# Optimization experiments

Measured on AMD Instinct MI355X. Metric: run time of the kernel, lower is better.

The kernel has to match this reference:

```python
import jax, jax.numpy as jnp
import numpy as np

N = 20000      # points
K = 16         # neighbor pairs per query per branch
M = N * K      # total pairs
C = 384        # embed_dim
H = 6          # num_heads
HD = C // H    # head_dim = 64
H1 = H // 2    # cartesian-branch heads
L = 24         # quant_grid_length (window 6.0 / quant 0.25)
Q = 0.25       # quant_size
LS = 24        # quant_grid_length_sphere (120 / 5)
QS = 5.0       # quant_size_sphere
A = 0.05 * 0.25  # exponential_split 'a'
SCALE = HD ** -0.5


def setup_inputs() -> dict:
    key = jax.random.key(0)
    ks = jax.random.split(key, 12)
    s = 0.02
    inp = {}
    inp["query_feats"] = jax.random.normal(ks[0], (N, C), jnp.float32)
    inp["xyz"] = jax.random.uniform(ks[1], (N, 3), jnp.float32, -3.0, 3.0)
    inp["index_0"] = jnp.repeat(jnp.arange(N, dtype=jnp.int32), K)
    inp["index_1"] = jax.random.randint(ks[2], (M,), 0, N, dtype=jnp.int32)
    inp["index_0_sphere"] = jnp.repeat(jnp.arange(N, dtype=jnp.int32), K)
    inp["index_1_sphere"] = jax.random.randint(ks[3], (M,), 0, N, dtype=jnp.int32)
    inp["W_qkv"] = jax.random.normal(ks[4], (C, 3 * C), jnp.float32) * s
    inp["b_qkv"] = jnp.zeros((3 * C,), jnp.float32)
    inp["W_proj"] = jax.random.normal(ks[5], (C, C), jnp.float32) * s
    inp["b_proj"] = jnp.zeros((C,), jnp.float32)
    inp["tq"] = jax.random.normal(ks[6], (2 * L - 1, 3, H1, HD), jnp.float32) * s
    inp["tk"] = jax.random.normal(ks[7], (2 * L - 1, 3, H1, HD), jnp.float32) * s
    inp["tv"] = jax.random.normal(ks[8], (2 * L - 1, 3, H1, HD), jnp.float32) * s
    inp["tq_s"] = jax.random.normal(ks[9], (2 * LS, 3, H - H1, HD), jnp.float32) * s
    inp["tk_s"] = jax.random.normal(ks[10], (2 * LS, 3, H - H1, HD), jnp.float32) * s
    inp["tv_s"] = jax.random.normal(ks[11], (2 * LS, 3, H - H1, HD), jnp.float32) * s
    return inp


def _cart2sphere(xyz):
    x, y, z = xyz[:, 0], xyz[:, 1], xyz[:, 2]
    theta = (jnp.arctan2(y, x) + np.pi) * (180.0 / np.pi)
    beta = jnp.arctan2(jnp.sqrt(x * x + y * y), z) * (180.0 / np.pi)
    r = jnp.sqrt(x * x + y * y + z * z)
    return jnp.stack([theta, beta, r], -1)


def _rel_idx_cart(xyz, i0, i1):
    rel = xyz[i0] - xyz[i1]  # [M,3]
    idx = jnp.floor(rel / Q).astype(jnp.int32) + (L - 1)
    return jnp.clip(idx, 0, 2 * L - 2)


def _rel_idx_sphere(sph, i0, i1):
    rel = sph[i0] - sph[i1]  # [M,3] (theta, beta, r)
    idx01 = jnp.clip(jnp.floor(rel[:, :2] / QS).astype(jnp.int32) + LS, 0, 2 * LS - 1)
    # exponential_split on radial dim
    r = rel[:, 2]
    ra = jnp.abs(r)
    flag = (r >= 0).astype(jnp.float32)
    idx = 2.0 * jnp.floor(jnp.log((ra + 2.0 * A) / A) / np.log(2.0)) - 2.0
    idx = idx + ((3.0 * jnp.exp2(jnp.floor(idx / 2.0)) - 2.0) * A <= ra).astype(jnp.float32)
    idx = idx * (2.0 * flag - 1.0) + (flag - 1.0)
    idx2 = jnp.clip(idx.astype(jnp.int32) + 24, 0, 2 * LS - 1)
    return jnp.concatenate([idx01, idx2[:, None]], 1)


def _branch(q, k, v, i0, i1, rel_idx, Tq, Tk, Tv):
    # q,k,v: [N,h,d]; i0/i1: [M]; rel_idx: [M,3]; tables: [R,3,h,d]
    qg = q[i0]  # [M,h,d]
    kg = k[i1]
    attn = jnp.einsum('mhd,mhd->mh', qg, kg)
    for dim in range(3):
        attn = attn + jnp.einsum('mhd,mhd->mh', qg, Tq[rel_idx[:, dim], dim])
        attn = attn + jnp.einsum('mhd,mhd->mh', kg, Tk[rel_idx[:, dim], dim])
    # segment softmax over queries (i0)
    seg_max = jax.ops.segment_max(attn, i0, num_segments=N)
    ex = jnp.exp(attn - seg_max[i0])
    p = ex / jax.ops.segment_sum(ex, i0, num_segments=N)[i0]  # [M,h]
    vg = v[i1] + Tv[rel_idx[:, 0], 0] + Tv[rel_idx[:, 1], 1] + Tv[rel_idx[:, 2], 2]
    return jax.ops.segment_sum(p[:, :, None] * vg, i0, num_segments=N)  # [N,h,d]


def reference(query_feats, xyz, index_0, index_1, index_0_sphere, index_1_sphere,
              W_qkv, b_qkv, W_proj, b_proj, tq, tk, tv, tq_s, tk_s, tv_s):
    i0 = index_0.astype(jnp.int32)
    i1 = index_1.astype(jnp.int32)
    i0s = index_0_sphere.astype(jnp.int32)
    i1s = index_1_sphere.astype(jnp.int32)
    qkv = (query_feats @ W_qkv + b_qkv).reshape(N, 3, H, HD)
    q = qkv[:, 0] * SCALE
    k = qkv[:, 1]
    v = qkv[:, 2]
    sph = _cart2sphere(xyz)
    ri = _rel_idx_cart(xyz, i0, i1)
    out1 = _branch(q[:, :H1], k[:, :H1], v[:, :H1], i0, i1, ri, tq, tk, tv)
    ri_s = _rel_idx_sphere(sph, i0s, i1s)
    out2 = _branch(q[:, H1:], k[:, H1:], v[:, H1:], i0s, i1s, ri_s, tq_s, tk_s, tv_s)
    x = jnp.concatenate([out1, out2], 1).reshape(N, C)
    return x @ W_proj + b_proj
```

## Files before the change

kernel.cpp:

```cpp
#include <hip/hip_runtime.h>
#include <hip/hip_bf16.h>

namespace {

constexpr int NP   = 20000;
constexpr int CD   = 384;
constexpr int QKVD = 1152;
constexpr int TC   = 47 * 3 * 3 * 64;
constexpr int TS   = 48 * 3 * 3 * 64;

constexpr int PB0 = NP * CD / 4 / 256;
constexpr int PB1 = PB0 + (QKVD / 32) * (CD / 32);
constexpr int PB2 = PB1 + (CD / 32) * (CD / 32);
constexpr int PB3 = PB2 + 27 * 7;

typedef __attribute__((ext_vector_type(8))) short short8;
typedef __attribute__((ext_vector_type(4))) float f32x4;
typedef __attribute__((ext_vector_type(2))) float f32x2;

__device__ inline float f32_atan2(float y, float x) {
  return (float)atan2((double)y, (double)x);
}
__device__ inline float f32_log(float x) {
  return (float)log((double)x);
}

__device__ inline float bfl(unsigned u) {
  union { unsigned u; float f; } c; c.u = u << 16; return c.f;
}
__device__ inline float bfh(unsigned u) {
  union { unsigned u; float f; } c; c.u = u & 0xffff0000u; return c.f;
}
__device__ inline f32x2 up2(unsigned u) {
  f32x2 r;
  r.x = bfl(u);
  r.y = bfh(u);
  return r;
}
__device__ inline unsigned short f2bf(float x) {
  __hip_bfloat16 hb = __float2bfloat16(x);
  unsigned short u; __builtin_memcpy(&u, &hb, 2);
  return u;
}

#if __has_builtin(__builtin_amdgcn_fdot2_f32_bf16)
#define HAVE_BF16_DOT 1
typedef __attribute__((ext_vector_type(2))) __bf16 bf16x2_t;
__device__ inline float dot2bf(unsigned a, unsigned b, float c) {
  bf16x2_t av, bv;
  __builtin_memcpy(&av, &a, 4);
  __builtin_memcpy(&bv, &b, 4);
  return __builtin_amdgcn_fdot2_f32_bf16(av, bv, c, false);
}
#endif

__device__ inline void async16(const void* g, void* l) {
  __builtin_amdgcn_global_load_lds(
      (const __attribute__((address_space(1))) unsigned int*)g,
      (__attribute__((address_space(3))) unsigned int*)l,
      16, 0, 0);
}

__global__ __launch_bounds__(256) void prep_all_k(const float* __restrict__ qf,
                                                  unsigned short* __restrict__ qf_b,
                                                  const float* __restrict__ Wqkv,
                                                  unsigned short* __restrict__ wqkvT,
                                                  const float* __restrict__ Wproj,
                                                  unsigned short* __restrict__ wprojT,
                                                  const float* __restrict__ tq,
                                                  const float* __restrict__ tk,
                                                  const float* __restrict__ tv,
                                                  const float* __restrict__ tqs,
                                                  const float* __restrict__ tks,
                                                  const float* __restrict__ tvs,
                                                  unsigned short* __restrict__ tq_b,
                                                  unsigned short* __restrict__ tk_b,
                                                  unsigned short* __restrict__ tv_b,
                                                  unsigned short* __restrict__ tqs_b,
                                                  unsigned short* __restrict__ tks_b,
                                                  unsigned short* __restrict__ tvs_b,
                                                  const float* __restrict__ xyz,
                                                  float* __restrict__ sph) {
  const int bid = blockIdx.x;
  const int tid = threadIdx.x;
  __shared__ float t[32][33];

  if (bid < PB0) {
    int i = (bid * 256 + tid) * 4;
    float4 v = *(const float4*)(qf + i);
    ushort4 o;
    o.x = f2bf(v.x); o.y = f2bf(v.y); o.z = f2bf(v.z); o.w = f2bf(v.w);
    *(ushort4*)(qf_b + i) = o;
  } else if (bid < PB2) {
    const float* in;
    unsigned short* out;
    int R, Cc, bx, by;
    if (bid < PB1) {
      in = Wqkv; out = wqkvT; R = CD; Cc = QKVD;
      int tt = bid - PB0; bx = tt % (QKVD / 32); by = tt / (QKVD / 32);
    } else {
      in = Wproj; out = wprojT; R = CD; Cc = CD;
      int tt = bid - PB1; bx = tt % (CD / 32); by = tt / (CD / 32);
    }
    const int c0 = bx * 32, r0 = by * 32;
    const int tx = tid & 31, ty = tid >> 5;
    #pragma unroll
    for (int i = 0; i < 32; i += 8)
      t[ty + i][tx] = in[(size_t)(r0 + ty + i) * Cc + (c0 + tx)];
    __syncthreads();
    #pragma unroll
    for (int i = 0; i < 32; i += 8)
      out[(size_t)(c0 + ty + i) * R + (r0 + tx)] = f2bf(t[tx][ty + i]);
  } else {
    const int tt = bid - PB2;
    const int bx = tt % 27, y = tt / 27;
    const int th = bx * 256 + tid;
    if (y < 6) {
      const float* in = (y == 0) ? tq : (y == 1) ? tk : (y == 2) ? tv
                      : (y == 3) ? tqs : (y == 4) ? tks : tvs;
      unsigned short* out = (y == 0) ? tq_b : (y == 1) ? tk_b : (y == 2) ? tv_b
                          : (y == 3) ? tqs_b : (y == 4) ? tks_b : tvs_b;
      const int n = (y < 3) ? TC : TS;
      int i = th * 4;
      if (i < n) {
        float4 v = *(const float4*)(in + i);
        ushort4 o;
        o.x = f2bf(v.x); o.y = f2bf(v.y); o.z = f2bf(v.z); o.w = f2bf(v.w);
        *(ushort4*)(out + i) = o;
      }
    } else {
#pragma clang fp contract(off)
      #pragma unroll
      for (int r = 0; r < 4; ++r) {
        int i = th * 4 + r;
        if (i < NP) {
          const float PIF = 3.14159265358979323846f;
          const float R2D = 57.29577951308232f;
          float x = xyz[i * 3 + 0], yy = xyz[i * 3 + 1], z = xyz[i * 3 + 2];
          float sxy = x * x + yy * yy;
          sph[i * 3 + 0] = (f32_atan2(yy, x) + PIF) * R2D;
          sph[i * 3 + 1] = f32_atan2(sqrtf(sxy), z) * R2D;
          sph[i * 3 + 2] = sqrtf(sxy + z * z);
        }
      }
    }
  }
}

template <int MODE>
__global__ __launch_bounds__(256) void gemm_async_k(const short* __restrict__ A,
                                                    const short* __restrict__ BT,
                                                    const float* __restrict__ bias,
                                                    void* __restrict__ Cout,
                                                    int M, int Nn, int K) {
  __shared__ short As[2][128][32];
  __shared__ short Bs[2][128][32];
  const int tid  = threadIdx.x;
  const int m0   = blockIdx.x * 128, n0 = blockIdx.y * 128;
  const int wave = tid >> 6, lane = tid & 63;
  const int wm   = (wave & 1) * 64, wn = (wave >> 1) * 64;
  const int quad = lane >> 4, l16 = lane & 15;
  const int srow = lane >> 2;
  const int scol = (lane & 3) * 8;

  f32x4 acc[4][4] = {};

  auto stage = [&](int buf, int k0) {
    #pragma unroll
    for (int c = 0; c < 2; ++c) {
      const int base = (wave + c * 4) * 16;
      async16(A + (size_t)(m0 + base + srow) * K + k0 + scol, &As[buf][base][0]);
      async16(BT + (size_t)(n0 + base + srow) * K + k0 + scol, &Bs[buf][base][0]);
    }
  };

  stage(0, 0);
  int cur = 0;
  for (int k0 = 0; k0 < K; k0 += 32) {
    if (k0 + 32 < K) {
      stage(cur ^ 1, k0 + 32);
      asm volatile("s_waitcnt vmcnt(4)" ::: "memory");
    } else {
      asm volatile("s_waitcnt vmcnt(0)" ::: "memory");
    }
    __builtin_amdgcn_s_barrier();
    short8 af[4], bg[4];
    #pragma unroll
    for (int i = 0; i < 4; ++i) af[i] = *(const short8*)&As[cur][wm + i * 16 + l16][quad * 8];
    #pragma unroll
    for (int j = 0; j < 4; ++j) bg[j] = *(const short8*)&Bs[cur][wn + j * 16 + l16][quad * 8];
    #pragma unroll
    for (int i = 0; i < 4; ++i)
      #pragma unroll
      for (int j = 0; j < 4; ++j)
        acc[i][j] = __builtin_amdgcn_mfma_f32_16x16x32_bf16(af[i], bg[j], acc[i][j], 0, 0, 0);
    __builtin_amdgcn_s_barrier();
    cur ^= 1;
  }

  #pragma unroll
  for (int i = 0; i < 4; ++i) {
    #pragma unroll
    for (int j = 0; j < 4; ++j) {
      int gn = n0 + wn + j * 16 + l16;
      if (gn >= Nn) continue;
      float bval = bias[gn];
      #pragma unroll
      for (int r = 0; r < 4; ++r) {
        int gm = m0 + wm + i * 16 + quad * 4 + r;
        if (gm < M) {
          float v = acc[i][j][r] + bval;
          if (MODE == 0) {
            if (gn < 384) v *= 0.125f;
            ((unsigned short*)Cout)[(size_t)gm * Nn + gn] = f2bf(v);
          } else {
            ((float*)Cout)[(size_t)gm * Nn + gn] = v;
          }
        }
      }
    }
  }
}

__device__ inline f32x2 dot8_pk(uint4 q, uint4 k, uint4 a0, uint4 a1, uint4 a2,
                                uint4 t0, uint4 t1, uint4 t2, f32x2 acc) {
  const unsigned* qp = &q.x;  const unsigned* kp = &k.x;
  const unsigned* a0p = &a0.x; const unsigned* a1p = &a1.x; const unsigned* a2p = &a2.x;
  const unsigned* t0p = &t0.x; const unsigned* t1p = &t1.x; const unsigned* t2p = &t2.x;
  #pragma unroll
  for (int w2 = 0; w2 < 4; ++w2) {
    f32x2 qf = up2(qp[w2]), kf = up2(kp[w2]);
    f32x2 tqs = up2(a0p[w2]) + up2(a1p[w2]) + up2(a2p[w2]);
    f32x2 tks = up2(t0p[w2]) + up2(t1p[w2]) + up2(t2p[w2]);
    acc += qf * (kf + tqs) + kf * tks;
  }
  return acc;
}

__device__ inline void acc4(f32x2* vc, uint4 vv, uint4 t0, uint4 t1, uint4 t2,
                            float pr) {
  f32x2 prv = {pr, pr};
  vc[0] += prv * (up2(vv.x) + up2(t0.x) + up2(t1.x) + up2(t2.x));
  vc[1] += prv * (up2(vv.y) + up2(t0.y) + up2(t1.y) + up2(t2.y));
  vc[2] += prv * (up2(vv.z) + up2(t0.z) + up2(t1.z) + up2(t2.z));
  vc[3] += prv * (up2(vv.w) + up2(t0.w) + up2(t1.w) + up2(t2.w));
}

__global__ __launch_bounds__(384, 5) void attn6_k(const unsigned short* __restrict__ qkv,
                                                  const float* __restrict__ xyz,
                                                  const float* __restrict__ sph,
                                                  const int* __restrict__ nb_c,
                                                  const int* __restrict__ nb_s,
                                                  const unsigned short* __restrict__ tq_c,
                                                  const unsigned short* __restrict__ tk_c,
                                                  const unsigned short* __restrict__ tv_c,
                                                  const unsigned short* __restrict__ tq_s,
                                                  const unsigned short* __restrict__ tk_s,
                                                  const unsigned short* __restrict__ tv_s,
                                                  unsigned short* __restrict__ xout) {
  __shared__ int   s_i1 [2][16];
  __shared__ int   s_off[2][16][3];
  __shared__ float s_p  [6][16];

  const int w    = threadIdx.x >> 6;
  const int lane = threadIdx.x & 63;
  const int n    = blockIdx.x;
  const int b    = (w >= 3) ? 1 : 0;
  const int hh   = w - b * 3;

  const unsigned short* tqb = b ? tq_s : tq_c;
  const unsigned short* tkb = b ? tk_s : tk_c;
  const unsigned short* tvb = b ? tv_s : tv_c;

  const int eg = lane >> 2, g = lane & 3;
  const int goff = g * 16;
  const unsigned short* qp = qkv + (size_t)n * QKVD + b * 192 + hh * 64 + goff;
  const uint4 qv0 = *(const uint4*)(qp);
  const uint4 qv1 = *(const uint4*)(qp + 8);

  if (lane < 16 && (w == 0 || w == 3)) {
#pragma clang fp contract(off)
    const int e = lane;
    if (b == 0) {
      const int i1 = nb_c[n * 16 + e];
      s_i1[0][e] = i1;
      const float rel[3] = {xyz[n * 3 + 0] - xyz[i1 * 3 + 0],
                            xyz[n * 3 + 1] - xyz[i1 * 3 + 1],
                            xyz[n * 3 + 2] - xyz[i1 * 3 + 2]};
      #pragma unroll
      for (int dim = 0; dim < 3; ++dim) {
        int idx = (int)floorf(rel[dim] * 4.0f) + 23;
        idx = min(max(idx, 0), 46);
        s_off[0][e][dim] = (idx * 3 + dim) * 192;
      }
    } else {
      const int i1 = nb_s[n * 16 + e];
      s_i1[1][e] = i1;
      const float d0 = sph[n * 3 + 0] - sph[i1 * 3 + 0];
      const float d1 = sph[n * 3 + 1] - sph[i1 * 3 + 1];
      const float dr = sph[n * 3 + 2] - sph[i1 * 3 + 2];
      int i0a = (int)floorf(d0 / 5.0f) + 24;
      int i1a = (int)floorf(d1 / 5.0f) + 24;
      const float ra = fabsf(dr);
      const float flag = (dr >= 0.0f) ? 1.0f : 0.0f;
      const float t = (ra + 0.025f) / 0.0125f;
      const float wv = f32_log(t) / 0.69314718055994531f;
      float fidx = 2.0f * floorf(wv) - 2.0f;
      fidx += ((3.0f * exp2f(floorf(fidx * 0.5f)) - 2.0f) * 0.0125f <= ra) ? 1.0f : 0.0f;
      fidx = fidx * (2.0f * flag - 1.0f) + (flag - 1.0f);
      int i2a = (int)fidx + 24;
      s_off[1][e][0] = (min(max(i0a, 0), 47) * 3 + 0) * 192;
      s_off[1][e][1] = (min(max(i1a, 0), 47) * 3 + 1) * 192;
      s_off[1][e][2] = (min(max(i2a, 0), 47) * 3 + 2) * 192;
    }
  }
  __syncthreads();

  float p;
  {
    const int i1 = s_i1[b][eg];
    const int o0 = s_off[b][eg][0] + hh * 64 + goff;
    const int o1 = s_off[b][eg][1] + hh * 64 + goff;
    const int o2 = s_off[b][eg][2] + hh * 64 + goff;
    const unsigned short* kp = qkv + (size_t)i1 * QKVD + 384 + b * 192 + hh * 64 + goff;
    uint4 kv0 = *(const uint4*)(kp);
    uint4 kv1 = *(const uint4*)(kp + 8);
    uint4 a00 = *(const uint4*)(tqb + o0);
    uint4 a01 = *(const uint4*)(tqb + o0 + 8);
    uint4 a10 = *(const uint4*)(tqb + o1);
    uint4 a11 = *(const uint4*)(tqb + o1 + 8);
    uint4 a20 = *(const uint4*)(tqb + o2);
    uint4 a21 = *(const uint4*)(tqb + o2 + 8);
    uint4 b00 = *(const uint4*)(tkb + o0);
    uint4 b01 = *(const uint4*)(tkb + o0 + 8);
    uint4 b10 = *(const uint4*)(tkb + o1);
    uint4 b11 = *(const uint4*)(tkb + o1 + 8);
    uint4 b20 = *(const uint4*)(tkb + o2);
    uint4 b21 = *(const uint4*)(tkb + o2 + 8);
    float acc;
#ifdef HAVE_BF16_DOT
    float aqk = 0.0f, aq0 = 0.0f, aq1 = 0.0f, aq2 = 0.0f;
    float ak0 = 0.0f, ak1 = 0.0f, ak2 = 0.0f;
#define DOT7(qd, kd, a0d, a1d, a2d, b0d, b1d, b2d)                         \
    aqk = dot2bf(qd, kd, aqk);  aq0 = dot2bf(qd, a0d, aq0);                \
    aq1 = dot2bf(qd, a1d, aq1); aq2 = dot2bf(qd, a2d, aq2);                \
    ak0 = dot2bf(kd, b0d, ak0); ak1 = dot2bf(kd, b1d, ak1);                \
    ak2 = dot2bf(kd, b2d, ak2);
    DOT7(qv0.x, kv0.x, a00.x, a10.x, a20.x, b00.x, b10.x, b20.x)
    DOT7(qv0.y, kv0.y, a00.y, a10.y, a20.y, b00.y, b10.y, b20.y)
    DOT7(qv0.z, kv0.z, a00.z, a10.z, a20.z, b00.z, b10.z, b20.z)
    DOT7(qv0.w, kv0.w, a00.w, a10.w, a20.w, b00.w, b10.w, b20.w)
    DOT7(qv1.x, kv1.x, a01.x, a11.x, a21.x, b01.x, b11.x, b21.x)
    DOT7(qv1.y, kv1.y, a01.y, a11.y, a21.y, b01.y, b11.y, b21.y)
    DOT7(qv1.z, kv1.z, a01.z, a11.z, a21.z, b01.z, b11.z, b21.z)
    DOT7(qv1.w, kv1.w, a01.w, a11.w, a21.w, b01.w, b11.w, b21.w)
#undef DOT7
    acc = ((aqk + aq0) + (aq1 + aq2)) + ((ak0 + ak1) + ak2);
#else
    f32x2 acc2 = {0.0f, 0.0f};
    acc2 = dot8_pk(qv0, kv0, a00, a10, a20, b00, b10, b20, acc2);
    acc2 = dot8_pk(qv1, kv1, a01, a11, a21, b01, b11, b21, acc2);
    acc = acc2.x + acc2.y;
#endif
    acc += __shfl_xor(acc, 1);
    acc += __shfl_xor(acc, 2);

    float m = acc;
    #pragma unroll
    for (int off = 4; off <= 32; off <<= 1) m = fmaxf(m, __shfl_xor(m, off));
    float ex = __expf(acc - m);
    float s = ex;
    #pragma unroll
    for (int off = 4; off <= 32; off <<= 1) s += __shfl_xor(s, off);
    p = ex / s;
    if (g == 0) s_p[w][eg] = p;
  }

  {
    const int e8 = lane >> 3;
    const int c  = lane & 7;
    const int hc = hh * 64 + c * 8;
    const int offVa = s_i1[b][e8]     * QKVD + 768 + b * 192 + hc;
    const int offVb = s_i1[b][e8 + 8] * QKVD + 768 + b * 192 + hc;
    const int offA0 = s_off[b][e8][0] + hc;
    const int offA1 = s_off[b][e8][1] + hc;
    const int offA2 = s_off[b][e8][2] + hc;
    const int offB0 = s_off[b][e8 + 8][0] + hc;
    const int offB1 = s_off[b][e8 + 8][1] + hc;
    const int offB2 = s_off[b][e8 + 8][2] + hc;

    uint4 vA  = *(const uint4*)(qkv + offVa);
    uint4 tA0 = *(const uint4*)(tvb + offA0);
    uint4 tA1 = *(const uint4*)(tvb + offA1);
    uint4 tA2 = *(const uint4*)(tvb + offA2);
    uint4 vB  = *(const uint4*)(qkv + offVb);
    uint4 tB0 = *(const uint4*)(tvb + offB0);
    uint4 tB1 = *(const uint4*)(tvb + offB1);
    uint4 tB2 = *(const uint4*)(tvb + offB2);

    f32x2 vc[4] = {{0.f, 0.f}, {0.f, 0.f}, {0.f, 0.f}, {0.f, 0.f}};
    acc4(vc, vA, tA0, tA1, tA2, s_p[w][e8]);
    acc4(vc, vB, tB0, tB1, tB2, s_p[w][e8 + 8]);

    #pragma unroll
    for (int q4 = 0; q4 < 4; ++q4) {
      #pragma unroll
      for (int off = 8; off <= 32; off <<= 1) {
        vc[q4].x += __shfl_xor(vc[q4].x, off);
        vc[q4].y += __shfl_xor(vc[q4].y, off);
      }
    }
    if (e8 == 0) {
      uint4 o;
      o.x = ((unsigned)f2bf(vc[0].y) << 16) | (unsigned)f2bf(vc[0].x);
      o.y = ((unsigned)f2bf(vc[1].y) << 16) | (unsigned)f2bf(vc[1].x);
      o.z = ((unsigned)f2bf(vc[2].y) << 16) | (unsigned)f2bf(vc[2].x);
      o.w = ((unsigned)f2bf(vc[3].y) << 16) | (unsigned)f2bf(vc[3].x);
      *(uint4*)(xout + (size_t)n * CD + (b * 3 + hh) * 64 + c * 8) = o;
    }
  }
}

}

extern "C" void kernel_launch(void* const* d_in, const int* in_sizes, int n_in,
                              void* d_out, int out_size, void* d_ws, size_t ws_size,
                              hipStream_t stream) {
  const float* qf    = (const float*)d_in[0];
  const float* xyz   = (const float*)d_in[1];
  const int*   i1c   = (const int*)d_in[3];
  const int*   i1s   = (const int*)d_in[5];
  const float* Wqkv  = (const float*)d_in[6];
  const float* bqkv  = (const float*)d_in[7];
  const float* Wproj = (const float*)d_in[8];
  const float* bproj = (const float*)d_in[9];
  const float* tq    = (const float*)d_in[10];
  const float* tk    = (const float*)d_in[11];
  const float* tv    = (const float*)d_in[12];
  const float* tqs   = (const float*)d_in[13];
  const float* tks   = (const float*)d_in[14];
  const float* tvs   = (const float*)d_in[15];

  char* w = (char*)d_ws;
  unsigned short* qf_b   = (unsigned short*)w; w += (size_t)NP * CD * 2;
  unsigned short* wqkvT  = (unsigned short*)w; w += (size_t)QKVD * CD * 2;
  unsigned short* wprojT = (unsigned short*)w; w += (size_t)CD * CD * 2;
  unsigned short* qkv_b  = (unsigned short*)w; w += (size_t)NP * QKVD * 2;
  unsigned short* x_b    = (unsigned short*)w; w += (size_t)NP * CD * 2;
  float*          sph    = (float*)w;          w += (size_t)NP * 3 * 4;
  unsigned short* tq_b   = (unsigned short*)w; w += (size_t)TC * 2;
  unsigned short* tk_b   = (unsigned short*)w; w += (size_t)TC * 2;
  unsigned short* tv_b   = (unsigned short*)w; w += (size_t)TC * 2;
  unsigned short* tqs_b  = (unsigned short*)w; w += (size_t)TS * 2;
  unsigned short* tks_b  = (unsigned short*)w; w += (size_t)TS * 2;
  unsigned short* tvs_b  = (unsigned short*)w;

  prep_all_k<<<PB3, 256, 0, stream>>>(qf, qf_b, Wqkv, wqkvT, Wproj, wprojT,
                                      tq, tk, tv, tqs, tks, tvs,
                                      tq_b, tk_b, tv_b, tqs_b, tks_b, tvs_b,
                                      xyz, sph);

  gemm_async_k<0><<<dim3((NP + 127) / 128, QKVD / 128), 256, 0, stream>>>(
      (const short*)qf_b, (const short*)wqkvT, bqkv, qkv_b, NP, QKVD, CD);

  attn6_k<<<NP, 384, 0, stream>>>(qkv_b, xyz, sph, i1c, i1s,
                                  tq_b, tk_b, tv_b, tqs_b, tks_b, tvs_b, x_b);

  gemm_async_k<1><<<dim3((NP + 127) / 128, CD / 128), 256, 0, stream>>>(
      (const short*)x_b, (const short*)wprojT, bproj, d_out, NP, CD, CD);
}
```

Before: 325.6 us.

## Stage per-head relative-position tables in swizzled LDS and precompute pair bins

Restructures the attention kernel so each block handles one (branch, head) pair over a range of nodes. The block loads that head's q/k/v relative-position tables into XOR-swizzled shared memory once and serves the table lookups from LDS instead of global memory. A new bin_k kernel precomputes each pair's bin indices and neighbor index into a buffer, and softmax probabilities are broadcast with shuffles rather than through shared memory. The cost is an extra kernel launch, a round trip for the bin buffer through global memory, a large LDS footprint per block, and q/k/v rows for one node now fetched by six separate blocks.

Measured after the change: 288.0 us. -11.6%, faster.

```diff
diff --git a/kernel.cpp b/kernel.cpp
--- a/kernel.cpp
+++ b/kernel.cpp
@@ -13,6 +13,9 @@
 constexpr int PB1 = PB0 + (QKVD / 32) * (CD / 32);
 constexpr int PB2 = PB1 + (CD / 32) * (CD / 32);
 constexpr int PB3 = PB2 + 27 * 7;
+
+constexpr int ANB = 240;
+constexpr int ANY = (NP + ANB - 1) / ANB;
 
 typedef __attribute__((ext_vector_type(8))) short short8;
 typedef __attribute__((ext_vector_type(4))) float f32x4;
@@ -59,6 +62,13 @@
       (const __attribute__((address_space(1))) unsigned int*)g,
       (__attribute__((address_space(3))) unsigned int*)l,
       16, 0, 0);
+}
+
+__device__ inline uint4 tld(const char* t, int row, int bo) {
+  return *(const uint4*)(t + row * 128 + (bo ^ ((row & 7) << 4)));
+}
+__device__ inline void tst(char* t, int row, int bo, uint4 v) {
+  *(uint4*)(t + row * 128 + (bo ^ ((row & 7) << 4))) = v;
 }
 
 __global__ __launch_bounds__(256) void prep_all_k(const float* __restrict__ qf,
@@ -147,6 +157,55 @@
   }
 }
 
+__global__ __launch_bounds__(256) void bin_k(const float* __restrict__ xyz,
+                                             const float* __restrict__ sph,
+                                             const int* __restrict__ nb_c,
+                                             const int* __restrict__ nb_s,
+                                             int4* __restrict__ ebuf) {
+#pragma clang fp contract(off)
+  const int t = blockIdx.x * 256 + threadIdx.x;
+  if (t >= 2 * NP * 16) return;
+  const int b   = t / (NP * 16);
+  const int rem = t - b * NP * 16;
+  const int n   = rem >> 4;
+  const int e   = rem & 15;
+  int4 o;
+  if (b == 0) {
+    const int i1 = nb_c[n * 16 + e];
+    const float rel[3] = {xyz[n * 3 + 0] - xyz[i1 * 3 + 0],
+                          xyz[n * 3 + 1] - xyz[i1 * 3 + 1],
+                          xyz[n * 3 + 2] - xyz[i1 * 3 + 2]};
+    int r[3];
+    #pragma unroll
+    for (int dim = 0; dim < 3; ++dim) {
+      int idx = (int)floorf(rel[dim] * 4.0f) + 23;
+      idx = min(max(idx, 0), 46);
+      r[dim] = idx * 3 + dim;
+    }
+    o.x = r[0]; o.y = r[1]; o.z = r[2]; o.w = i1;
+  } else {
+    const int i1 = nb_s[n * 16 + e];
+    const float d0 = sph[n * 3 + 0] - sph[i1 * 3 + 0];
+    const float d1 = sph[n * 3 + 1] - sph[i1 * 3 + 1];
+    const float dr = sph[n * 3 + 2] - sph[i1 * 3 + 2];
+    int i0a = (int)floorf(d0 / 5.0f) + 24;
+    int i1a = (int)floorf(d1 / 5.0f) + 24;
+    const float ra = fabsf(dr);
+    const float flag = (dr >= 0.0f) ? 1.0f : 0.0f;
+    const float tt = (ra + 0.025f) / 0.0125f;
+    const float wv = f32_log(tt) / 0.69314718055994531f;
+    float fidx = 2.0f * floorf(wv) - 2.0f;
+    fidx += ((3.0f * exp2f(floorf(fidx * 0.5f)) - 2.0f) * 0.0125f <= ra) ? 1.0f : 0.0f;
+    fidx = fidx * (2.0f * flag - 1.0f) + (flag - 1.0f);
+    int i2a = (int)fidx + 24;
+    o.x = min(max(i0a, 0), 47) * 3 + 0;
+    o.y = min(max(i1a, 0), 47) * 3 + 1;
+    o.z = min(max(i2a, 0), 47) * 3 + 2;
+    o.w = i1;
+  }
+  ebuf[t] = o;
+}
+
 template <int MODE>
 __global__ __launch_bounds__(256) void gemm_async_k(const short* __restrict__ A,
                                                     const short* __restrict__ BT,
@@ -246,97 +305,68 @@
   vc[3] += prv * (up2(vv.w) + up2(t0.w) + up2(t1.w) + up2(t2.w));
 }
 
-__global__ __launch_bounds__(384, 5) void attn6_k(const unsigned short* __restrict__ qkv,
-                                                  const float* __restrict__ xyz,
-                                                  const float* __restrict__ sph,
-                                                  const int* __restrict__ nb_c,
-                                                  const int* __restrict__ nb_s,
-                                                  const unsigned short* __restrict__ tq_c,
-                                                  const unsigned short* __restrict__ tk_c,
-                                                  const unsigned short* __restrict__ tv_c,
-                                                  const unsigned short* __restrict__ tq_s,
-                                                  const unsigned short* __restrict__ tk_s,
-                                                  const unsigned short* __restrict__ tv_s,
-                                                  unsigned short* __restrict__ xout) {
-  __shared__ int   s_i1 [2][16];
-  __shared__ int   s_off[2][16][3];
-  __shared__ float s_p  [6][16];
-
-  const int w    = threadIdx.x >> 6;
-  const int lane = threadIdx.x & 63;
-  const int n    = blockIdx.x;
-  const int b    = (w >= 3) ? 1 : 0;
-  const int hh   = w - b * 3;
-
-  const unsigned short* tqb = b ? tq_s : tq_c;
-  const unsigned short* tkb = b ? tk_s : tk_c;
-  const unsigned short* tvb = b ? tv_s : tv_c;
+__global__ __launch_bounds__(512, 4) void attn_lds_k(const unsigned short* __restrict__ qkv,
+                                                     const int4* __restrict__ ebuf,
+                                                     const unsigned short* __restrict__ tq_c,
+                                                     const unsigned short* __restrict__ tk_c,
+                                                     const unsigned short* __restrict__ tv_c,
+                                                     const unsigned short* __restrict__ tq_s,
+                                                     const unsigned short* __restrict__ tk_s,
+                                                     const unsigned short* __restrict__ tv_s,
+                                                     unsigned short* __restrict__ xout) {
+  __shared__ char s_tq[144 * 128];
+  __shared__ char s_tk[144 * 128];
+  __shared__ char s_tv[144 * 128];
+
+  const int bh  = blockIdx.x;
+  const int b   = bh / 3;
+  const int hh  = bh % 3;
+  const int wid = threadIdx.x >> 6, lane = threadIdx.x & 63;
+
+  const unsigned short* gtq = b ? tq_s : tq_c;
+  const unsigned short* gtk = b ? tk_s : tk_c;
+  const unsigned short* gtv = b ? tv_s : tv_c;
+  const int nrows = b ? 144 : 141;
+
+  for (int i = threadIdx.x; i < nrows * 8; i += 512) {
+    const int row = i >> 3, c8 = i & 7;
+    const int go = row * 192 + hh * 64 + c8 * 8;
+    tst(s_tq, row, c8 * 16, *(const uint4*)(gtq + go));
+    tst(s_tk, row, c8 * 16, *(const uint4*)(gtk + go));
+    tst(s_tv, row, c8 * 16, *(const uint4*)(gtv + go));
+  }
+  __syncthreads();
 
   const int eg = lane >> 2, g = lane & 3;
-  const int goff = g * 16;
-  const unsigned short* qp = qkv + (size_t)n * QKVD + b * 192 + hh * 64 + goff;
-  const uint4 qv0 = *(const uint4*)(qp);
-  const uint4 qv1 = *(const uint4*)(qp + 8);
-
-  if (lane < 16 && (w == 0 || w == 3)) {
-#pragma clang fp contract(off)
-    const int e = lane;
-    if (b == 0) {
-      const int i1 = nb_c[n * 16 + e];
-      s_i1[0][e] = i1;
-      const float rel[3] = {xyz[n * 3 + 0] - xyz[i1 * 3 + 0],
-                            xyz[n * 3 + 1] - xyz[i1 * 3 + 1],
-                            xyz[n * 3 + 2] - xyz[i1 * 3 + 2]};
-      #pragma unroll
-      for (int dim = 0; dim < 3; ++dim) {
-        int idx = (int)floorf(rel[dim] * 4.0f) + 23;
-        idx = min(max(idx, 0), 46);
-        s_off[0][e][dim] = (idx * 3 + dim) * 192;
-      }
-    } else {
-      const int i1 = nb_s[n * 16 + e];
-      s_i1[1][e] = i1;
-      const float d0 = sph[n * 3 + 0] - sph[i1 * 3 + 0];
-      const float d1 = sph[n * 3 + 1] - sph[i1 * 3 + 1];
-      const float dr = sph[n * 3 + 2] - sph[i1 * 3 + 2];
-      int i0a = (int)floorf(d0 / 5.0f) + 24;
-      int i1a = (int)floorf(d1 / 5.0f) + 24;
-      const float ra = fabsf(dr);
-      const float flag = (dr >= 0.0f) ? 1.0f : 0.0f;
-      const float t = (ra + 0.025f) / 0.0125f;
-      const float wv = f32_log(t) / 0.69314718055994531f;
-      float fidx = 2.0f * floorf(wv) - 2.0f;
-      fidx += ((3.0f * exp2f(floorf(fidx * 0.5f)) - 2.0f) * 0.0125f <= ra) ? 1.0f : 0.0f;
-      fidx = fidx * (2.0f * flag - 1.0f) + (flag - 1.0f);
-      int i2a = (int)fidx + 24;
-      s_off[1][e][0] = (min(max(i0a, 0), 47) * 3 + 0) * 192;
-      s_off[1][e][1] = (min(max(i1a, 0), 47) * 3 + 1) * 192;
-      s_off[1][e][2] = (min(max(i2a, 0), 47) * 3 + 2) * 192;
-    }
-  }
-  __syncthreads();
-
-  float p;
-  {
-    const int i1 = s_i1[b][eg];
-    const int o0 = s_off[b][eg][0] + hh * 64 + goff;
-    const int o1 = s_off[b][eg][1] + hh * 64 + goff;
-    const int o2 = s_off[b][eg][2] + hh * 64 + goff;
-    const unsigned short* kp = qkv + (size_t)i1 * QKVD + 384 + b * 192 + hh * 64 + goff;
-    uint4 kv0 = *(const uint4*)(kp);
-    uint4 kv1 = *(const uint4*)(kp + 8);
-    uint4 a00 = *(const uint4*)(tqb + o0);
-    uint4 a01 = *(const uint4*)(tqb + o0 + 8);
-    uint4 a10 = *(const uint4*)(tqb + o1);
-    uint4 a11 = *(const uint4*)(tqb + o1 + 8);
-    uint4 a20 = *(const uint4*)(tqb + o2);
-    uint4 a21 = *(const uint4*)(tqb + o2 + 8);
-    uint4 b00 = *(const uint4*)(tkb + o0);
-    uint4 b01 = *(const uint4*)(tkb + o0 + 8);
-    uint4 b10 = *(const uint4*)(tkb + o1);
-    uint4 b11 = *(const uint4*)(tkb + o1 + 8);
-    uint4 b20 = *(const uint4*)(tkb + o2);
-    uint4 b21 = *(const uint4*)(tkb + o2 + 8);
+  const int e8 = lane >> 3, c = lane & 7;
+  const int node_end = min(blockIdx.y * ANB + ANB, NP);
+
+  for (int node = blockIdx.y * ANB + wid; node < node_end; node += 8) {
+    const int4* eb = ebuf + ((size_t)b * NP + node) * 16;
+
+    const int4 E  = eb[eg];
+    const int4 EA = eb[e8];
+    const int4 EB = eb[e8 + 8];
+
+    const unsigned short* qp = qkv + (size_t)node * QKVD + b * 192 + hh * 64 + g * 16;
+    const uint4 qv0 = *(const uint4*)(qp);
+    const uint4 qv1 = *(const uint4*)(qp + 8);
+    const unsigned short* kp = qkv + (size_t)E.w * QKVD + 384 + b * 192 + hh * 64 + g * 16;
+    const uint4 kv0 = *(const uint4*)(kp);
+    const uint4 kv1 = *(const uint4*)(kp + 8);
+    const unsigned short* vpA = qkv + (size_t)EA.w * QKVD + 768 + b * 192 + hh * 64 + c * 8;
+    const unsigned short* vpB = qkv + (size_t)EB.w * QKVD + 768 + b * 192 + hh * 64 + c * 8;
+    const uint4 vA = *(const uint4*)(vpA);
+    const uint4 vB = *(const uint4*)(vpB);
+
+    const int bo = g * 32;
+    const uint4 a00 = tld(s_tq, E.x, bo), a01 = tld(s_tq, E.x, bo + 16);
+    const uint4 a10 = tld(s_tq, E.y, bo), a11 = tld(s_tq, E.y, bo + 16);
+    const uint4 a20 = tld(s_tq, E.z, bo), a21 = tld(s_tq, E.z, bo + 16);
+    const uint4 b00 = tld(s_tk, E.x, bo), b01 = tld(s_tk, E.x, bo + 16);
+    const uint4 b10 = tld(s_tk, E.y, bo), b11 = tld(s_tk, E.y, bo + 16);
+    const uint4 b20 = tld(s_tk, E.z, bo), b21 = tld(s_tk, E.z, bo + 16);
+
     float acc;
 #ifdef HAVE_BF16_DOT
     float aqk = 0.0f, aq0 = 0.0f, aq1 = 0.0f, aq2 = 0.0f;
@@ -372,35 +402,21 @@
     float s = ex;
     #pragma unroll
     for (int off = 4; off <= 32; off <<= 1) s += __shfl_xor(s, off);
-    p = ex / s;
-    if (g == 0) s_p[w][eg] = p;
-  }
-
-  {
-    const int e8 = lane >> 3;
-    const int c  = lane & 7;
-    const int hc = hh * 64 + c * 8;
-    const int offVa = s_i1[b][e8]     * QKVD + 768 + b * 192 + hc;
-    const int offVb = s_i1[b][e8 + 8] * QKVD + 768 + b * 192 + hc;
-    const int offA0 = s_off[b][e8][0] + hc;
-    const int offA1 = s_off[b][e8][1] + hc;
-    const int offA2 = s_off[b][e8][2] + hc;
-    const int offB0 = s_off[b][e8 + 8][0] + hc;
-    const int offB1 = s_off[b][e8 + 8][1] + hc;
-    const int offB2 = s_off[b][e8 + 8][2] + hc;
-
-    uint4 vA  = *(const uint4*)(qkv + offVa);
-    uint4 tA0 = *(const uint4*)(tvb + offA0);
-    uint4 tA1 = *(const uint4*)(tvb + offA1);
-    uint4 tA2 = *(const uint4*)(tvb + offA2);
-    uint4 vB  = *(const uint4*)(qkv + offVb);
-    uint4 tB0 = *(const uint4*)(tvb + offB0);
-    uint4 tB1 = *(const uint4*)(tvb + offB1);
-    uint4 tB2 = *(const uint4*)(tvb + offB2);
+    const float p = ex / s;
+
+    const float pA = __shfl(p, e8 << 2);
+    const float pB = __shfl(p, (e8 + 8) << 2);
+    const int vbo = c * 16;
+    const uint4 tA0 = tld(s_tv, EA.x, vbo);
+    const uint4 tA1 = tld(s_tv, EA.y, vbo);
+    const uint4 tA2 = tld(s_tv, EA.z, vbo);
+    const uint4 tB0 = tld(s_tv, EB.x, vbo);
+    const uint4 tB1 = tld(s_tv, EB.y, vbo);
+    const uint4 tB2 = tld(s_tv, EB.z, vbo);
 
     f32x2 vc[4] = {{0.f, 0.f}, {0.f, 0.f}, {0.f, 0.f}, {0.f, 0.f}};
-    acc4(vc, vA, tA0, tA1, tA2, s_p[w][e8]);
-    acc4(vc, vB, tB0, tB1, tB2, s_p[w][e8 + 8]);
+    acc4(vc, vA, tA0, tA1, tA2, pA);
+    acc4(vc, vB, tB0, tB1, tB2, pB);
 
     #pragma unroll
     for (int q4 = 0; q4 < 4; ++q4) {
@@ -416,7 +432,7 @@
       o.y = ((unsigned)f2bf(vc[1].y) << 16) | (unsigned)f2bf(vc[1].x);
       o.z = ((unsigned)f2bf(vc[2].y) << 16) | (unsigned)f2bf(vc[2].x);
       o.w = ((unsigned)f2bf(vc[3].y) << 16) | (unsigned)f2bf(vc[3].x);
-      *(uint4*)(xout + (size_t)n * CD + (b * 3 + hh) * 64 + c * 8) = o;
+      *(uint4*)(xout + (size_t)node * CD + (b * 3 + hh) * 64 + c * 8) = o;
     }
   }
 }
@@ -453,18 +469,22 @@
   unsigned short* tv_b   = (unsigned short*)w; w += (size_t)TC * 2;
   unsigned short* tqs_b  = (unsigned short*)w; w += (size_t)TS * 2;
   unsigned short* tks_b  = (unsigned short*)w; w += (size_t)TS * 2;
-  unsigned short* tvs_b  = (unsigned short*)w;
+  unsigned short* tvs_b  = (unsigned short*)w; w += (size_t)TS * 2;
+  int4*           ebuf   = (int4*)w;
 
   prep_all_k<<<PB3, 256, 0, stream>>>(qf, qf_b, Wqkv, wqkvT, Wproj, wprojT,
                                       tq, tk, tv, tqs, tks, tvs,
                                       tq_b, tk_b, tv_b, tqs_b, tks_b, tvs_b,
                                       xyz, sph);
 
+  bin_k<<<(2 * NP * 16 + 255) / 256, 256, 0, stream>>>(xyz, sph, i1c, i1s, ebuf);
+
   gemm_async_k<0><<<dim3((NP + 127) / 128, QKVD / 128), 256, 0, stream>>>(
       (const short*)qf_b, (const short*)wqkvT, bqkv, qkv_b, NP, QKVD, CD);
 
-  attn6_k<<<NP, 384, 0, stream>>>(qkv_b, xyz, sph, i1c, i1s,
-                                  tq_b, tk_b, tv_b, tqs_b, tks_b, tvs_b, x_b);
+  attn_lds_k<<<dim3(6, ANY), 512, 0, stream>>>(qkv_b, ebuf,
+                                               tq_b, tk_b, tv_b,
+                                               tqs_b, tks_b, tvs_b, x_b);
 
   gemm_async_k<1><<<dim3((NP + 127) / 128, CD / 128), 256, 0, stream>>>(
       (const short*)x_b, (const short*)wprojT, bproj, d_out, NP, CD, CD);
```
